# Performance work log

Measured on AMD Instinct MI355X. Metric: run time of the kernel, lower is better.

Reference implementation:

```python
import jax, jax.numpy as jnp
import numpy as np

B, S, D, A, E = 32, 2048, 512, 64, 64
EPS = 1e-5

def setup_inputs() -> dict:
    key = jax.random.key(0)
    ks = jax.random.split(key, 12)
    sc = 0.02
    return {
        "source_embedding": jax.random.normal(ks[0], (B, E), jnp.float32),
        "inputs": jax.random.normal(ks[1], (B, S, D), jnp.float32),
        "down_w_W": sc * jax.random.normal(ks[2], (E, A * D), jnp.float32),
        "down_w_b": jnp.zeros((A * D,), jnp.float32),
        "down_b_W": sc * jax.random.normal(ks[3], (E, A), jnp.float32),
        "down_b_b": jnp.zeros((A,), jnp.float32),
        "up_w_W": sc * jax.random.normal(ks[4], (E, D * A), jnp.float32),
        "up_w_b": jnp.zeros((D * A,), jnp.float32),
        "up_b_W": sc * jax.random.normal(ks[5], (E, D), jnp.float32),
        "up_b_b": jnp.zeros((D,), jnp.float32),
        "pre_w_W": sc * jax.random.normal(ks[6], (E, D), jnp.float32),
        "pre_w_b": jnp.ones((D,), jnp.float32),
        "pre_b_W": sc * jax.random.normal(ks[7], (E, D), jnp.float32),
        "pre_b_b": jnp.zeros((D,), jnp.float32),
        "post_w_W": sc * jax.random.normal(ks[8], (E, D), jnp.float32),
        "post_w_b": jnp.ones((D,), jnp.float32),
        "post_b_W": sc * jax.random.normal(ks[9], (E, D), jnp.float32),
        "post_b_b": jnp.zeros((D,), jnp.float32),
    }

def _cond_ln(x, w, b):
    # x: [B,S,D]; w,b: [B,D] -> per-sample affine layernorm over last dim
    mean = jnp.mean(x, axis=2, keepdims=True)
    var = jnp.mean((x - mean) ** 2, axis=2, keepdims=True) + EPS
    return (x - mean) / jnp.sqrt(var) * w[:, None, :] + b[:, None, :]

def reference(source_embedding, inputs,
              down_w_W, down_w_b, down_b_W, down_b_b,
              up_w_W, up_w_b, up_b_W, up_b_b,
              pre_w_W, pre_w_b, pre_b_W, pre_b_b,
              post_w_W, post_w_b, post_b_W, post_b_b):
    emb = source_embedding  # [B,E]
    # hypernet-generated per-sample adapter weights
    w_down = (emb @ down_w_W + down_w_b).reshape(B, A, D)  # [B,A,D]
    b_down = emb @ down_b_W + down_b_b                      # [B,A]
    w_up = (emb @ up_w_W + up_w_b).reshape(B, D, A)         # [B,D,A]
    b_up = emb @ up_b_W + up_b_b                            # [B,D]
    # conditional pre layernorm
    pre_w = emb @ pre_w_W + pre_w_b
    pre_b = emb @ pre_b_W + pre_b_b
    z = _cond_ln(inputs, pre_w, pre_b)
    # adapter: down-proj, relu, up-proj (matmul with weight.transpose(1,2))
    down = jnp.einsum('bsd,bad->bsa', z, w_down) + b_down[:, None, :]
    mid = jax.nn.relu(down)
    out = jnp.einsum('bsa,bda->bsd', mid, w_up) + b_up[:, None, :]
    # conditional post layernorm
    post_w = emb @ post_w_W + post_w_b
    post_b = emb @ post_b_W + post_b_b
    out = _cond_ln(out, post_w, post_b)
    return out + inputs
```

## Files before the change

### kernel.cpp

```cpp
#include <hip/hip_runtime.h>

#define NB 32
#define NS 2048
#define ND 512
#define NA 64
#define NE 64

typedef __bf16 bf16x8 __attribute__((ext_vector_type(8)));
typedef float f32x4 __attribute__((ext_vector_type(4)));

__device__ __forceinline__ unsigned short f2bf(float f) {
    union { float f; unsigned u; } v; v.f = f;
    unsigned r = (v.u + 0x7fffu + ((v.u >> 16) & 1u)) >> 16;
    return (unsigned short)r;
}

__global__ __launch_bounds__(256) void hyper_pack(
    const float* __restrict__ emb,
    const float* __restrict__ dwW, const float* __restrict__ dwb,
    const float* __restrict__ uwW, const float* __restrict__ uwb,
    unsigned short* __restrict__ wdfrag, unsigned short* __restrict__ wufrag) {
    __shared__ float Wt[64][256];
    __shared__ float embs[NB * NE];
    const int tid = threadIdx.x;
    const int bx = blockIdx.x;
    const int mat = bx >> 7;
    const int chunk = bx & 127;
    const int base = chunk * 256;
    const float* W = mat ? uwW : dwW;
    const float* bias = mat ? uwb : dwb;

    for (int i = tid; i < NB * NE; i += 256) embs[i] = emb[i];
    for (int k = 0; k < 64; ++k) Wt[k][tid] = W[(size_t)k * 32768 + base + tid];
    __syncthreads();

    const int col = base + tid;
    const float bv = bias[col];
    float acc[NB];
#pragma unroll
    for (int b = 0; b < NB; ++b) acc[b] = bv;

    for (int k0 = 0; k0 < 64; k0 += 4) {
        float w0 = Wt[k0][tid], w1 = Wt[k0 + 1][tid];
        float w2 = Wt[k0 + 2][tid], w3 = Wt[k0 + 3][tid];
#pragma unroll
        for (int b = 0; b < NB; ++b) {
            float4 e = *(const float4*)&embs[b * 64 + k0];
            acc[b] = fmaf(e.x, w0, acc[b]);
            acc[b] = fmaf(e.y, w1, acc[b]);
            acc[b] = fmaf(e.z, w2, acc[b]);
            acc[b] = fmaf(e.w, w3, acc[b]);
        }
    }

    if (mat == 0) {
        int a = col >> 9, d = col & 511;
        size_t idx0 = ((size_t)((a >> 4) * 16 + (d >> 5)) * 64 +
                       (((d & 31) >> 3) * 16 + (a & 15))) * 8 + (d & 7);
#pragma unroll
        for (int b = 0; b < NB; ++b) wdfrag[idx0 + (size_t)b * 32768] = f2bf(acc[b]);
    } else {
        int d = col >> 6, a = col & 63;
        size_t idx0 = ((size_t)((d >> 4) * 2 + (a >> 5)) * 64 +
                       (((a & 31) >> 3) * 16 + (d & 15))) * 8 + (a & 7);
#pragma unroll
        for (int b = 0; b < NB; ++b) wufrag[idx0 + (size_t)b * 32768] = f2bf(acc[b]);
    }
}

__global__ __launch_bounds__(256) void hyper_vec(
    const float* __restrict__ emb,
    const float* __restrict__ pwW, const float* __restrict__ pwb,
    const float* __restrict__ pbW, const float* __restrict__ pbb,
    const float* __restrict__ powW, const float* __restrict__ powb,
    const float* __restrict__ pobW, const float* __restrict__ pobb,
    const float* __restrict__ ubW, const float* __restrict__ ubb,
    const float* __restrict__ dbW, const float* __restrict__ dbb,
    float* __restrict__ vecs) {
    int gid = blockIdx.x * 256 + threadIdx.x;
    if (gid >= NB * 2624) return;
    int b = gid / 2624;
    int r = gid - b * 2624;
    const float* W; const float* bias; int off, width;
    if (r < 2560) {
        int v = r >> 9; off = r & 511; width = 512;
        switch (v) {
            case 0:  W = pwW;  bias = pwb;  break;
            case 1:  W = pbW;  bias = pbb;  break;
            case 2:  W = powW; bias = powb; break;
            case 3:  W = pobW; bias = pobb; break;
            default: W = ubW;  bias = ubb;  break;
        }
    } else {
        off = r - 2560; width = 64; W = dbW; bias = dbb;
    }
    float acc = bias[off];
    const float* e = emb + b * 64;
#pragma unroll 8
    for (int k = 0; k < 64; ++k) acc = fmaf(e[k], W[k * width + off], acc);
    vecs[gid] = acc;
}

__global__ __launch_bounds__(256, 2) void fused_adapter(
    const float* __restrict__ inp,
    const unsigned short* __restrict__ wdfrag,
    const unsigned short* __restrict__ wufrag,
    const float* __restrict__ vecs,
    float* __restrict__ out) {
    __shared__ unsigned short z_lds[64][520];
    __shared__ unsigned short mid_lds[64][72];

    const int tid = threadIdx.x;
    const int lane = tid & 63;
    const int wave = tid >> 6;
    const int lanelo = lane & 15;
    const int quad = lane >> 4;
    const int bx = blockIdx.x;
    const int b = bx >> 5;
    const int s0 = (bx & 31) * 64;

    const float* vb = vecs + b * 2624;
    const float* pre_w  = vb;
    const float* pre_b  = vb + 512;
    const float* post_w = vb + 1024;
    const float* post_b = vb + 1536;
    const float* b_up   = vb + 2048;
    const float* b_down = vb + 2560;

    const float* xblk = inp + ((size_t)(b * NS + s0)) * ND;

    const int d0 = lane * 4;
    const float4 pw0 = *(const float4*)(pre_w + d0);
    const float4 pw1 = *(const float4*)(pre_w + 256 + d0);
    const float4 pb0 = *(const float4*)(pre_b + d0);
    const float4 pb1 = *(const float4*)(pre_b + 256 + d0);

    for (int r = wave; r < 64; r += 4) {
        const float* xp = xblk + (size_t)r * ND;
        float4 x0 = *(const float4*)(xp + d0);
        float4 x1 = *(const float4*)(xp + 256 + d0);
        float s = x0.x + x0.y + x0.z + x0.w + x1.x + x1.y + x1.z + x1.w;
        float q = x0.x * x0.x + x0.y * x0.y + x0.z * x0.z + x0.w * x0.w +
                  x1.x * x1.x + x1.y * x1.y + x1.z * x1.z + x1.w * x1.w;
#pragma unroll
        for (int m = 1; m <= 32; m <<= 1) {
            s += __shfl_xor(s, m);
            q += __shfl_xor(q, m);
        }
        float mean = s * (1.0f / 512.0f);
        float var = q * (1.0f / 512.0f) - mean * mean;
        float rstd = rsqrtf(var + 1e-5f);
        float z0 = (x0.x - mean) * rstd * pw0.x + pb0.x;
        float z1 = (x0.y - mean) * rstd * pw0.y + pb0.y;
        float z2 = (x0.z - mean) * rstd * pw0.z + pb0.z;
        float z3 = (x0.w - mean) * rstd * pw0.w + pb0.w;
        float z4 = (x1.x - mean) * rstd * pw1.x + pb1.x;
        float z5 = (x1.y - mean) * rstd * pw1.y + pb1.y;
        float z6 = (x1.z - mean) * rstd * pw1.z + pb1.z;
        float z7 = (x1.w - mean) * rstd * pw1.w + pb1.w;
        unsigned lo0 = (unsigned)f2bf(z0) | ((unsigned)f2bf(z1) << 16);
        unsigned hi0 = (unsigned)f2bf(z2) | ((unsigned)f2bf(z3) << 16);
        unsigned lo1 = (unsigned)f2bf(z4) | ((unsigned)f2bf(z5) << 16);
        unsigned hi1 = (unsigned)f2bf(z6) | ((unsigned)f2bf(z7) << 16);
        *(uint2*)&z_lds[r][d0] = make_uint2(lo0, hi0);
        *(uint2*)&z_lds[r][256 + d0] = make_uint2(lo1, hi1);
    }
    __syncthreads();

    const int m0 = wave * 16;
    const unsigned short* wd = wdfrag + (size_t)b * 32768;
    f32x4 accd[4];
#pragma unroll
    for (int nt = 0; nt < 4; ++nt) accd[nt] = (f32x4){0.f, 0.f, 0.f, 0.f};
    const int arow = m0 + lanelo;
#pragma unroll
    for (int kc = 0; kc < 16; ++kc) {
        uint4 au = *(const uint4*)&z_lds[arow][kc * 32 + quad * 8];
        bf16x8 af = __builtin_bit_cast(bf16x8, au);
#pragma unroll
        for (int nt = 0; nt < 4; ++nt) {
            uint4 bu = *(const uint4*)(wd + (size_t)((nt * 16 + kc) * 64 + lane) * 8);
            bf16x8 bf = __builtin_bit_cast(bf16x8, bu);
            accd[nt] = __builtin_amdgcn_mfma_f32_16x16x32_bf16(af, bf, accd[nt], 0, 0, 0);
        }
    }
#pragma unroll
    for (int nt = 0; nt < 4; ++nt) {
        float bd = b_down[nt * 16 + lanelo];
#pragma unroll
        for (int r = 0; r < 4; ++r) {
            float v = fmaxf(accd[nt][r] + bd, 0.0f);
            mid_lds[m0 + quad * 4 + r][nt * 16 + lanelo] = f2bf(v);
        }
    }
    __syncthreads();

    uint4 a0u = *(const uint4*)&mid_lds[m0 + lanelo][quad * 8];
    uint4 a1u = *(const uint4*)&mid_lds[m0 + lanelo][32 + quad * 8];
    bf16x8 af0 = __builtin_bit_cast(bf16x8, a0u);
    bf16x8 af1 = __builtin_bit_cast(bf16x8, a1u);
    const unsigned short* wu = wufrag + (size_t)b * 32768;
    f32x4 acc[32];
#pragma unroll
    for (int nt = 0; nt < 32; ++nt) acc[nt] = (f32x4){0.f, 0.f, 0.f, 0.f};
#pragma unroll
    for (int nt = 0; nt < 32; ++nt) {
        uint4 b0u = *(const uint4*)(wu + (size_t)((nt * 2 + 0) * 64 + lane) * 8);
        uint4 b1u = *(const uint4*)(wu + (size_t)((nt * 2 + 1) * 64 + lane) * 8);
        acc[nt] = __builtin_amdgcn_mfma_f32_16x16x32_bf16(af0, __builtin_bit_cast(bf16x8, b0u), acc[nt], 0, 0, 0);
        acc[nt] = __builtin_amdgcn_mfma_f32_16x16x32_bf16(af1, __builtin_bit_cast(bf16x8, b1u), acc[nt], 0, 0, 0);
    }

    float sum[4] = {0.f, 0.f, 0.f, 0.f}, sq[4] = {0.f, 0.f, 0.f, 0.f};
#pragma unroll
    for (int nt = 0; nt < 32; ++nt) {
        float bu = b_up[nt * 16 + lanelo];
#pragma unroll
        for (int r = 0; r < 4; ++r) {
            float v = acc[nt][r] + bu;
            acc[nt][r] = v;
            sum[r] += v;
            sq[r] += v * v;
        }
    }
#pragma unroll
    for (int r = 0; r < 4; ++r) {
#pragma unroll
        for (int m = 1; m <= 8; m <<= 1) {
            sum[r] += __shfl_xor(sum[r], m);
            sq[r] += __shfl_xor(sq[r], m);
        }
    }
    float mean[4], rstd[4];
#pragma unroll
    for (int r = 0; r < 4; ++r) {
        mean[r] = sum[r] * (1.0f / 512.0f);
        float var = sq[r] * (1.0f / 512.0f) - mean[r] * mean[r];
        rstd[r] = rsqrtf(var + 1e-5f);
    }

    const float* xwave = xblk + (size_t)m0 * ND;
    float* owave = out + ((size_t)(b * NS + s0 + m0)) * ND;
#pragma unroll
    for (int nt = 0; nt < 32; ++nt) {
        int col = nt * 16 + lanelo;
        float w = post_w[col], bb = post_b[col];
#pragma unroll
        for (int r = 0; r < 4; ++r) {
            size_t off = (size_t)(quad * 4 + r) * ND + col;
            owave[off] = (acc[nt][r] - mean[r]) * rstd[r] * w + bb + xwave[off];
        }
    }
}

extern "C" void kernel_launch(void* const* d_in, const int* in_sizes, int n_in,
                              void* d_out, int out_size, void* d_ws, size_t ws_size,
                              hipStream_t stream) {
    const float* emb  = (const float*)d_in[0];
    const float* inp  = (const float*)d_in[1];
    const float* dwW  = (const float*)d_in[2];
    const float* dwb  = (const float*)d_in[3];
    const float* dbW  = (const float*)d_in[4];
    const float* dbb  = (const float*)d_in[5];
    const float* uwW  = (const float*)d_in[6];
    const float* uwb  = (const float*)d_in[7];
    const float* ubW  = (const float*)d_in[8];
    const float* ubb  = (const float*)d_in[9];
    const float* pwW  = (const float*)d_in[10];
    const float* pwb  = (const float*)d_in[11];
    const float* pbW  = (const float*)d_in[12];
    const float* pbb  = (const float*)d_in[13];
    const float* powW = (const float*)d_in[14];
    const float* powb = (const float*)d_in[15];
    const float* pobW = (const float*)d_in[16];
    const float* pobb = (const float*)d_in[17];

    unsigned short* wdfrag = (unsigned short*)d_ws;
    unsigned short* wufrag = wdfrag + (size_t)NB * 32768;
    float* vecs = (float*)(wufrag + (size_t)NB * 32768);

    hyper_pack<<<256, 256, 0, stream>>>(emb, dwW, dwb, uwW, uwb, wdfrag, wufrag);
    hyper_vec<<<(NB * 2624 + 255) / 256, 256, 0, stream>>>(
        emb, pwW, pwb, pbW, pbb, powW, powb, pobW, pobb, ubW, ubb, dbW, dbb, vecs);
    fused_adapter<<<NB * (NS / 64), 256, 0, stream>>>(
        inp, wdfrag, wufrag, vecs, (float*)d_out);
}
```

Before: 338.3 us.

## Fold pre-LayerNorm affine into down weights and recompute up-proj to cut registers

A new hyper_c kernel folds the per-sample pre-LN scale into the down-projection weights and precomputes per-column constants. The main kernel can then feed raw bf16 inputs straight into the MFMA and apply mean/rstd after the matmul, which removes the z staging buffer in LDS and a block barrier. The up-projection MFMAs are run twice, once for the LN statistics and once for the output, instead of holding 32 accumulator tiles in registers. The adapter block also shrinks to 32 rows and 128 threads for higher occupancy, at the cost of doubled up-proj MFMA and weight loads and a different rounding point (raw x is rounded to bf16 before centering).

```diff
diff --git a/kernel.cpp b/kernel.cpp
--- a/kernel.cpp
+++ b/kernel.cpp
@@ -13,6 +13,15 @@
     union { float f; unsigned u; } v; v.f = f;
     unsigned r = (v.u + 0x7fffu + ((v.u >> 16) & 1u)) >> 16;
     return (unsigned short)r;
+}
+__device__ __forceinline__ unsigned pk(float a, float b) {
+    return (unsigned)f2bf(a) | ((unsigned)f2bf(b) << 16);
+}
+__device__ __forceinline__ float bflo(unsigned u) {
+    return __builtin_bit_cast(float, u << 16);
+}
+__device__ __forceinline__ float bfhi(unsigned u) {
+    return __builtin_bit_cast(float, u & 0xffff0000u);
 }
 
 __global__ __launch_bounds__(256) void hyper_pack(
@@ -31,7 +40,10 @@
     const float* bias = mat ? uwb : dwb;
 
     for (int i = tid; i < NB * NE; i += 256) embs[i] = emb[i];
-    for (int k = 0; k < 64; ++k) Wt[k][tid] = W[(size_t)k * 32768 + base + tid];
+    for (int i = tid; i < 64 * 64; i += 256) {
+        int k = i >> 6, c = (i & 63) << 2;
+        *(float4*)&Wt[k][c] = *(const float4*)&W[(size_t)k * 32768 + base + c];
+    }
     __syncthreads();
 
     const int col = base + tid;
@@ -101,14 +113,59 @@
     vecs[gid] = acc;
 }
 
-__global__ __launch_bounds__(256, 2) void fused_adapter(
+__global__ __launch_bounds__(256) void hyper_c(
+    unsigned short* __restrict__ wdfrag,
+    const float* __restrict__ vecs,
+    float* __restrict__ cvec) {
+    const int tid = threadIdx.x;
+    const int lane = tid & 63;
+    const int nblk = tid >> 6;
+    const int lanelo = lane & 15;
+    const int quad = lane >> 4;
+    const int b = blockIdx.x;
+    const float* vb = vecs + b * 2624;
+    unsigned short* wdb = wdfrag + (size_t)b * 32768;
+
+    float c1 = 0.f, c2 = 0.f;
+#pragma unroll
+    for (int kc = 0; kc < 16; ++kc) {
+        size_t off = ((size_t)(nblk * 16 + kc) * 64 + lane) * 8;
+        uint4 u = *(const uint4*)(wdb + off);
+        int d0 = kc * 32 + quad * 8;
+        float4 pwA = *(const float4*)(vb + d0);
+        float4 pwB = *(const float4*)(vb + d0 + 4);
+        float4 pbA = *(const float4*)(vb + 512 + d0);
+        float4 pbB = *(const float4*)(vb + 512 + d0 + 4);
+        float r0 = bflo(u.x), r1 = bfhi(u.x), r2 = bflo(u.y), r3 = bfhi(u.y);
+        float r4 = bflo(u.z), r5 = bfhi(u.z), r6 = bflo(u.w), r7 = bfhi(u.w);
+        float f0 = r0 * pwA.x, f1 = r1 * pwA.y, f2 = r2 * pwA.z, f3 = r3 * pwA.w;
+        float f4 = r4 * pwB.x, f5 = r5 * pwB.y, f6 = r6 * pwB.z, f7 = r7 * pwB.w;
+        c2 += (f0 + f1 + f2 + f3) + (f4 + f5 + f6 + f7);
+        c1 += r0 * pbA.x + r1 * pbA.y + r2 * pbA.z + r3 * pbA.w +
+              r4 * pbB.x + r5 * pbB.y + r6 * pbB.z + r7 * pbB.w;
+        uint4 o;
+        o.x = pk(f0, f1); o.y = pk(f2, f3); o.z = pk(f4, f5); o.w = pk(f6, f7);
+        *(uint4*)(wdb + off) = o;
+    }
+    c1 += __shfl_xor(c1, 16); c1 += __shfl_xor(c1, 32);
+    c2 += __shfl_xor(c2, 16); c2 += __shfl_xor(c2, 32);
+    if (quad == 0) {
+        int a = nblk * 16 + lanelo;
+        float c1p = c1 + vb[2560 + a];
+        cvec[b * 128 + 2 * a] = c1p;
+        cvec[b * 128 + 2 * a + 1] = c2;
+    }
+}
+
+__global__ __launch_bounds__(128, 5) void fused_adapter(
     const float* __restrict__ inp,
-    const unsigned short* __restrict__ wdfrag,
+    const unsigned short* __restrict__ wdfold,
     const unsigned short* __restrict__ wufrag,
     const float* __restrict__ vecs,
+    const float* __restrict__ cvec,
     float* __restrict__ out) {
-    __shared__ unsigned short z_lds[64][520];
-    __shared__ unsigned short mid_lds[64][72];
+    __shared__ float coeff[1536];
+    __shared__ __align__(16) unsigned short mid_lds[2][16][80];
 
     const int tid = threadIdx.x;
     const int lane = tid & 63;
@@ -116,111 +173,86 @@
     const int lanelo = lane & 15;
     const int quad = lane >> 4;
     const int bx = blockIdx.x;
-    const int b = bx >> 5;
-    const int s0 = (bx & 31) * 64;
+    const int b = bx >> 6;
+    const int s0 = (bx & 63) * 32;
+    const int m0 = wave * 16;
 
     const float* vb = vecs + b * 2624;
-    const float* pre_w  = vb;
-    const float* pre_b  = vb + 512;
-    const float* post_w = vb + 1024;
-    const float* post_b = vb + 1536;
-    const float* b_up   = vb + 2048;
-    const float* b_down = vb + 2560;
-
-    const float* xblk = inp + ((size_t)(b * NS + s0)) * ND;
-
-    const int d0 = lane * 4;
-    const float4 pw0 = *(const float4*)(pre_w + d0);
-    const float4 pw1 = *(const float4*)(pre_w + 256 + d0);
-    const float4 pb0 = *(const float4*)(pre_b + d0);
-    const float4 pb1 = *(const float4*)(pre_b + 256 + d0);
-
-    for (int r = wave; r < 64; r += 4) {
-        const float* xp = xblk + (size_t)r * ND;
-        float4 x0 = *(const float4*)(xp + d0);
-        float4 x1 = *(const float4*)(xp + 256 + d0);
-        float s = x0.x + x0.y + x0.z + x0.w + x1.x + x1.y + x1.z + x1.w;
-        float q = x0.x * x0.x + x0.y * x0.y + x0.z * x0.z + x0.w * x0.w +
-                  x1.x * x1.x + x1.y * x1.y + x1.z * x1.z + x1.w * x1.w;
-#pragma unroll
-        for (int m = 1; m <= 32; m <<= 1) {
-            s += __shfl_xor(s, m);
-            q += __shfl_xor(q, m);
-        }
-        float mean = s * (1.0f / 512.0f);
-        float var = q * (1.0f / 512.0f) - mean * mean;
-        float rstd = rsqrtf(var + 1e-5f);
-        float z0 = (x0.x - mean) * rstd * pw0.x + pb0.x;
-        float z1 = (x0.y - mean) * rstd * pw0.y + pb0.y;
-        float z2 = (x0.z - mean) * rstd * pw0.z + pb0.z;
-        float z3 = (x0.w - mean) * rstd * pw0.w + pb0.w;
-        float z4 = (x1.x - mean) * rstd * pw1.x + pb1.x;
-        float z5 = (x1.y - mean) * rstd * pw1.y + pb1.y;
-        float z6 = (x1.z - mean) * rstd * pw1.z + pb1.z;
-        float z7 = (x1.w - mean) * rstd * pw1.w + pb1.w;
-        unsigned lo0 = (unsigned)f2bf(z0) | ((unsigned)f2bf(z1) << 16);
-        unsigned hi0 = (unsigned)f2bf(z2) | ((unsigned)f2bf(z3) << 16);
-        unsigned lo1 = (unsigned)f2bf(z4) | ((unsigned)f2bf(z5) << 16);
-        unsigned hi1 = (unsigned)f2bf(z6) | ((unsigned)f2bf(z7) << 16);
-        *(uint2*)&z_lds[r][d0] = make_uint2(lo0, hi0);
-        *(uint2*)&z_lds[r][256 + d0] = make_uint2(lo1, hi1);
-    }
+    for (int i = tid; i < 384; i += 128)
+        ((float4*)coeff)[i] = ((const float4*)(vb + 1024))[i];
     __syncthreads();
 
-    const int m0 = wave * 16;
-    const unsigned short* wd = wdfrag + (size_t)b * 32768;
+    const float* xp = inp + ((size_t)b * NS + s0 + m0 + lanelo) * ND + quad * 8;
+    const unsigned short* wd = wdfold + (size_t)b * 32768;
     f32x4 accd[4];
 #pragma unroll
     for (int nt = 0; nt < 4; ++nt) accd[nt] = (f32x4){0.f, 0.f, 0.f, 0.f};
-    const int arow = m0 + lanelo;
+    float s = 0.f, q = 0.f;
 #pragma unroll
     for (int kc = 0; kc < 16; ++kc) {
-        uint4 au = *(const uint4*)&z_lds[arow][kc * 32 + quad * 8];
+        float4 x0 = *(const float4*)(xp + kc * 32);
+        float4 x1 = *(const float4*)(xp + kc * 32 + 4);
+        s += (x0.x + x0.y + x0.z + x0.w) + (x1.x + x1.y + x1.z + x1.w);
+        q = fmaf(x0.x, x0.x, q); q = fmaf(x0.y, x0.y, q);
+        q = fmaf(x0.z, x0.z, q); q = fmaf(x0.w, x0.w, q);
+        q = fmaf(x1.x, x1.x, q); q = fmaf(x1.y, x1.y, q);
+        q = fmaf(x1.z, x1.z, q); q = fmaf(x1.w, x1.w, q);
+        uint4 au;
+        au.x = pk(x0.x, x0.y); au.y = pk(x0.z, x0.w);
+        au.z = pk(x1.x, x1.y); au.w = pk(x1.z, x1.w);
         bf16x8 af = __builtin_bit_cast(bf16x8, au);
 #pragma unroll
         for (int nt = 0; nt < 4; ++nt) {
-            uint4 bu = *(const uint4*)(wd + (size_t)((nt * 16 + kc) * 64 + lane) * 8);
-            bf16x8 bf = __builtin_bit_cast(bf16x8, bu);
-            accd[nt] = __builtin_amdgcn_mfma_f32_16x16x32_bf16(af, bf, accd[nt], 0, 0, 0);
-        }
-    }
+            uint4 bu = *(const uint4*)(wd + ((size_t)(nt * 16 + kc) * 64 + lane) * 8);
+            accd[nt] = __builtin_amdgcn_mfma_f32_16x16x32_bf16(
+                af, __builtin_bit_cast(bf16x8, bu), accd[nt], 0, 0, 0);
+        }
+    }
+    s += __shfl_xor(s, 16); s += __shfl_xor(s, 32);
+    q += __shfl_xor(q, 16); q += __shfl_xor(q, 32);
+    float mean = s * (1.0f / 512.0f);
+    float var = q * (1.0f / 512.0f) - mean * mean;
+    float rstd = rsqrtf(var + 1e-5f);
+
+    float rs[4], mrs[4];
+#pragma unroll
+    for (int r = 0; r < 4; ++r) {
+        int src = quad * 4 + r;
+        rs[r] = __shfl(rstd, src);
+        mrs[r] = __shfl(mean, src) * rs[r];
+    }
+
+    const float* cv = cvec + b * 128;
 #pragma unroll
     for (int nt = 0; nt < 4; ++nt) {
-        float bd = b_down[nt * 16 + lanelo];
+        float2 cc = *(const float2*)(cv + 2 * (nt * 16 + lanelo));
 #pragma unroll
         for (int r = 0; r < 4; ++r) {
-            float v = fmaxf(accd[nt][r] + bd, 0.0f);
-            mid_lds[m0 + quad * 4 + r][nt * 16 + lanelo] = f2bf(v);
-        }
-    }
-    __syncthreads();
-
-    uint4 a0u = *(const uint4*)&mid_lds[m0 + lanelo][quad * 8];
-    uint4 a1u = *(const uint4*)&mid_lds[m0 + lanelo][32 + quad * 8];
+            float v = fmaf(rs[r], accd[nt][r], fmaf(-mrs[r], cc.y, cc.x));
+            v = fmaxf(v, 0.0f);
+            mid_lds[wave][quad * 4 + r][nt * 16 + lanelo] = f2bf(v);
+        }
+    }
+    uint4 a0u = *(const uint4*)&mid_lds[wave][lanelo][quad * 8];
+    uint4 a1u = *(const uint4*)&mid_lds[wave][lanelo][32 + quad * 8];
     bf16x8 af0 = __builtin_bit_cast(bf16x8, a0u);
     bf16x8 af1 = __builtin_bit_cast(bf16x8, a1u);
+
     const unsigned short* wu = wufrag + (size_t)b * 32768;
-    f32x4 acc[32];
-#pragma unroll
-    for (int nt = 0; nt < 32; ++nt) acc[nt] = (f32x4){0.f, 0.f, 0.f, 0.f};
+    float sum[4] = {0.f, 0.f, 0.f, 0.f}, sq[4] = {0.f, 0.f, 0.f, 0.f};
 #pragma unroll
     for (int nt = 0; nt < 32; ++nt) {
-        uint4 b0u = *(const uint4*)(wu + (size_t)((nt * 2 + 0) * 64 + lane) * 8);
-        uint4 b1u = *(const uint4*)(wu + (size_t)((nt * 2 + 1) * 64 + lane) * 8);
-        acc[nt] = __builtin_amdgcn_mfma_f32_16x16x32_bf16(af0, __builtin_bit_cast(bf16x8, b0u), acc[nt], 0, 0, 0);
-        acc[nt] = __builtin_amdgcn_mfma_f32_16x16x32_bf16(af1, __builtin_bit_cast(bf16x8, b1u), acc[nt], 0, 0, 0);
-    }
-
-    float sum[4] = {0.f, 0.f, 0.f, 0.f}, sq[4] = {0.f, 0.f, 0.f, 0.f};
-#pragma unroll
-    for (int nt = 0; nt < 32; ++nt) {
-        float bu = b_up[nt * 16 + lanelo];
+        uint4 b0 = *(const uint4*)(wu + ((size_t)(nt * 2 + 0) * 64 + lane) * 8);
+        uint4 b1 = *(const uint4*)(wu + ((size_t)(nt * 2 + 1) * 64 + lane) * 8);
+        f32x4 a4 = (f32x4){0.f, 0.f, 0.f, 0.f};
+        a4 = __builtin_amdgcn_mfma_f32_16x16x32_bf16(af0, __builtin_bit_cast(bf16x8, b0), a4, 0, 0, 0);
+        a4 = __builtin_amdgcn_mfma_f32_16x16x32_bf16(af1, __builtin_bit_cast(bf16x8, b1), a4, 0, 0, 0);
+        float bu = coeff[1024 + nt * 16 + lanelo];
 #pragma unroll
         for (int r = 0; r < 4; ++r) {
-            float v = acc[nt][r] + bu;
-            acc[nt][r] = v;
-            sum[r] += v;
-            sq[r] += v * v;
+            float y = a4[r] + bu;
+            sum[r] += y;
+            sq[r] = fmaf(y, y, sq[r]);
         }
     }
 #pragma unroll
@@ -231,24 +263,31 @@
             sq[r] += __shfl_xor(sq[r], m);
         }
     }
-    float mean[4], rstd[4];
+    float mean2[4], rstd2[4];
 #pragma unroll
     for (int r = 0; r < 4; ++r) {
-        mean[r] = sum[r] * (1.0f / 512.0f);
-        float var = sq[r] * (1.0f / 512.0f) - mean[r] * mean[r];
-        rstd[r] = rsqrtf(var + 1e-5f);
-    }
-
-    const float* xwave = xblk + (size_t)m0 * ND;
-    float* owave = out + ((size_t)(b * NS + s0 + m0)) * ND;
+        mean2[r] = sum[r] * (1.0f / 512.0f);
+        float v2 = sq[r] * (1.0f / 512.0f) - mean2[r] * mean2[r];
+        rstd2[r] = rsqrtf(v2 + 1e-5f);
+    }
+
+    const size_t obase = ((size_t)b * NS + s0 + m0) * ND;
 #pragma unroll
     for (int nt = 0; nt < 32; ++nt) {
+        uint4 b0 = *(const uint4*)(wu + ((size_t)(nt * 2 + 0) * 64 + lane) * 8);
+        uint4 b1 = *(const uint4*)(wu + ((size_t)(nt * 2 + 1) * 64 + lane) * 8);
+        f32x4 a4 = (f32x4){0.f, 0.f, 0.f, 0.f};
+        a4 = __builtin_amdgcn_mfma_f32_16x16x32_bf16(af0, __builtin_bit_cast(bf16x8, b0), a4, 0, 0, 0);
+        a4 = __builtin_amdgcn_mfma_f32_16x16x32_bf16(af1, __builtin_bit_cast(bf16x8, b1), a4, 0, 0, 0);
         int col = nt * 16 + lanelo;
-        float w = post_w[col], bb = post_b[col];
+        float bu = coeff[1024 + col];
+        float pw = coeff[col];
+        float pb = coeff[512 + col];
 #pragma unroll
         for (int r = 0; r < 4; ++r) {
-            size_t off = (size_t)(quad * 4 + r) * ND + col;
-            owave[off] = (acc[nt][r] - mean[r]) * rstd[r] * w + bb + xwave[off];
+            float y = a4[r] + bu;
+            size_t off = obase + (size_t)(quad * 4 + r) * ND + col;
+            out[off] = fmaf((y - mean2[r]) * rstd2[r], pw, pb) + inp[off];
         }
     }
 }
@@ -278,10 +317,12 @@
     unsigned short* wdfrag = (unsigned short*)d_ws;
     unsigned short* wufrag = wdfrag + (size_t)NB * 32768;
     float* vecs = (float*)(wufrag + (size_t)NB * 32768);
+    float* cvec = vecs + (size_t)NB * 2624;
 
     hyper_pack<<<256, 256, 0, stream>>>(emb, dwW, dwb, uwW, uwb, wdfrag, wufrag);
     hyper_vec<<<(NB * 2624 + 255) / 256, 256, 0, stream>>>(
         emb, pwW, pwb, pbW, pbb, powW, powb, pobW, pobb, ubW, ubb, dbW, dbb, vecs);
-    fused_adapter<<<NB * (NS / 64), 256, 0, stream>>>(
-        inp, wdfrag, wufrag, vecs, (float*)d_out);
-}
+    hyper_c<<<NB, 256, 0, stream>>>(wdfrag, vecs, cvec);
+    fused_adapter<<<NB * (NS / 32), 128, 0, stream>>>(
+        inp, wdfrag, wufrag, vecs, cvec, (float*)d_out);
+}
```

Result: slower. 429.4 us (+26.9%).
